# Kernel tuning notes

Measured on AMD Instinct MI355X. Metric: run time of the kernel, lower is better.

## Reference

```python
import jax, jax.numpy as jnp
from jax import lax
import numpy as np

# ---- dims / neuron params (match init_kwargs) ----
B, T, ENC, HID = 256, 500, 700, 128
TAU_MEM = 20.0      # tauSr == tauRef == tau_mem
THETA = 1.0         # spike_threshold
SCALE_REF = 1.0
WIDTH_GRAD = 1.0    # tauRho (surrogate width)
SCALE_GRAD = 1.0    # scaleRho (surrogate scale)


def alpha_filter(x, tau, mult):
    """Causal convolution along axis 0 with SLAYER's alpha (SRM) kernel
    h[k] = mult * (k/tau) * exp(1 - k/tau), Ts = 1.  Implemented as an exact
    2-state linear recurrence instead of an O(T^2) FIR conv.
    x: (T, ...) -> y: (T, ...)
    """
    d = jnp.exp(-1.0 / tau)          # per-step decay
    c = mult * jnp.exp(1.0) / tau    # h[k] = c * k * d**k

    def step(carry, xt):
        p, q = carry
        qn = d * q + c * d * p       # output at t (h[0] = 0)
        pn = d * p + xt
        return (pn, qn), qn

    z = jnp.zeros_like(x[0])
    _, y = lax.scan(step, (z, z), x)
    return y


def _spike_core(u):
    """SLAYER getSpikes: at each t, membrane = psp + accumulated refractory
    response (alpha kernel with mult = -2*theta*scaleRef, tau = tauRef) of all
    past spikes; emit spike (1/Ts) when membrane >= theta.
    u: (T, B, C) psp values -> (spikes, post-refractory membrane), both (T, B, C).
    """
    d = jnp.exp(-1.0 / TAU_MEM)
    c = (-2.0 * THETA * SCALE_REF) * jnp.exp(1.0) / TAU_MEM

    def step(carry, ut):
        p, q = carry
        qn = d * q + c * d * p       # refractory contribution at t (0 from spike at t)
        u_t = ut + qn                # membrane after refractory subtraction
        s_t = (u_t >= THETA).astype(ut.dtype)
        pn = d * p + s_t
        return (pn, qn), (s_t, u_t)

    z = jnp.zeros_like(u[0])
    _, (s, u_post) = lax.scan(step, (z, z), u)
    return s, u_post


@jax.custom_vjp
def spike(u):
    return _spike_core(u)[0]


def _spike_fwd(u):
    s, u_post = _spike_core(u)
    return s, u_post


def _spike_bwd(u_post, g):
    # SLAYER surrogate: pdf = scaleRho / (tauRho*theta) * exp(-|u - theta| / (tauRho*theta)),
    # evaluated on the refractory-modified membrane; grad does not flow through
    # the refractory recurrence (matches the torch autograd.Function).
    tc = WIDTH_GRAD * THETA
    pdf = (SCALE_GRAD / tc) * jnp.exp(-jnp.abs(u_post - THETA) / tc)
    return (g * pdf,)


spike.defvjp(_spike_fwd, _spike_bwd)


def setup_inputs():
    key = jax.random.key(0)
    k1, k2, k3 = jax.random.split(key, 3)
    # sparse binary input spike trains (B, T, ENC)
    x = (jax.random.uniform(k1, (B, T, ENC)) < 0.05).astype(jnp.float32)
    w1 = jax.random.normal(k2, (HID, ENC), dtype=jnp.float32) * 0.1
    w2 = jax.random.normal(k3, (1, HID), dtype=jnp.float32) * 0.3
    return {"x": x, "w1": w1, "w2": w2}


def reference(x, w1, w2):
    # x: (B, T, ENC) -> time-major (T, B, ENC) for the temporal scans
    xt = jnp.transpose(x, (1, 0, 2))
    h = jnp.einsum('tbc,hc->tbh', xt, w1)        # slayer.dense (bias-free linear per step)
    h = alpha_filter(h, TAU_MEM, 1.0)            # slayer.psp
    s1 = spike(h)                                # slayer.spike (threshold + refractory)
    o = jnp.einsum('tbh,oh->tbo', s1, w2)
    o = alpha_filter(o, TAU_MEM, 1.0)
    s2 = spike(o)
    return jnp.transpose(s2, (1, 0, 2))          # (B, T, 1), matches out2.movedim(-1, 1)
```

## Files before the change

### kernel.cpp

```cpp
#include <hip/hip_runtime.h>

#define BB  256
#define TT  500
#define ENC 700
#define ENC_PAD 704
#define HID 128
#define LMAX 80

__global__ __launch_bounds__(128) void transpose_w1_kernel(const float* __restrict__ w1,
                                                           float* __restrict__ w1t) {
    int c = blockIdx.x;
    int h = threadIdx.x;
    w1t[c * HID + h] = (c < ENC) ? w1[h * ENC + c] : 0.0f;
}

__global__ __launch_bounds__(256) void compress_kernel(const float* __restrict__ x,
                                                       ushort* __restrict__ lists,
                                                       int* __restrict__ ncnt) {
    __shared__ ushort lds[4][LMAX];
    const int lane = threadIdx.x & 63;
    const int w = threadIdx.x >> 6;
    const int r = blockIdx.x * 4 + w;
    const float* xrow = x + (size_t)r * ENC;
    const unsigned long long lt = (1ull << lane) - 1ull;

    float xv[11];
    #pragma unroll
    for (int k = 0; k < 11; ++k) {
        int c = k * 64 + lane;
        xv[k] = (c < ENC) ? xrow[c] : 0.0f;
    }
    int base = 0;
    #pragma unroll
    for (int k = 0; k < 11; ++k) {
        bool act = (xv[k] != 0.0f);
        unsigned long long m = __ballot(act);
        if (act) {
            int pos = base + (int)__popcll(m & lt);
            if (pos < LMAX) lds[w][pos] = (ushort)(k * 64 + lane);
        }
        base += (int)__popcll(m);
    }
    int n = (base < LMAX) ? base : LMAX;
    for (int p = n + lane; p < LMAX; p += 64) lds[w][p] = (ushort)ENC;
    if (lane == 0) ncnt[r] = n;
    if (lane < LMAX / 2)
        ((uint*)lists)[(size_t)r * (LMAX / 2) + lane] =
            ((const uint*)lds)[w * (LMAX / 2) + lane];
}

#define GROWS 512
#define GRP   64
#define QCH   16
#define WST   18

__global__ __launch_bounds__(256) void gather_kernel(const ushort* __restrict__ lists,
                                                     const int* __restrict__ ncnt,
                                                     const float* __restrict__ w1t,
                                                     float* __restrict__ h) {
    __shared__ float  w1q[ENC_PAD * WST];
    __shared__ ushort ll[GRP * LMAX];
    __shared__ int    nb[GRP];

    const int tid = threadIdx.x;
    const int lane = tid & 63;
    const int w = tid >> 6;
    const int q = blockIdx.y;
    const int r0b = blockIdx.x * GROWS;

    for (int i = tid; i < ENC_PAD * QCH; i += 256) {
        int c = i >> 4, ch = i & 15;
        w1q[c * WST + ch] = w1t[c * HID + q * QCH + ch];
    }

    const int chl = (lane & 7) * 2;
    const int rw  = lane >> 3;

    for (int g = 0; g < GROWS / GRP; ++g) {
        const int r0 = r0b + g * GRP;
        __syncthreads();
        {
            const uint* src = (const uint*)lists + (size_t)r0 * (LMAX / 2);
            uint* dst = (uint*)ll;
            #pragma unroll
            for (int k = 0; k < 10; ++k) dst[tid + k * 256] = src[tid + k * 256];
        }
        if (tid < GRP) nb[tid] = ncnt[r0 + tid];
        __syncthreads();

        #pragma unroll
        for (int p = 0; p < 2; ++p) {
            const int rl = p * 32 + w * 8 + rw;
            int n = nb[rl];
            n = max(n, __shfl_xor(n, 8));
            n = max(n, __shfl_xor(n, 16));
            n = max(n, __shfl_xor(n, 32));
            const int jmax = (n + 7) & ~7;

            float a0 = 0.f, a1 = 0.f;
            for (int j = 0; j < jmax; j += 8) {
                uint4 iv = *(const uint4*)&ll[rl * LMAX + j];
                int c0 = (int)(iv.x & 0xffff), c1 = (int)(iv.x >> 16);
                int c2 = (int)(iv.y & 0xffff), c3 = (int)(iv.y >> 16);
                int c4 = (int)(iv.z & 0xffff), c5 = (int)(iv.z >> 16);
                int c6 = (int)(iv.w & 0xffff), c7 = (int)(iv.w >> 16);
                float2 v0 = *(const float2*)&w1q[c0 * WST + chl];
                float2 v1 = *(const float2*)&w1q[c1 * WST + chl];
                float2 v2 = *(const float2*)&w1q[c2 * WST + chl];
                float2 v3 = *(const float2*)&w1q[c3 * WST + chl];
                float2 v4 = *(const float2*)&w1q[c4 * WST + chl];
                float2 v5 = *(const float2*)&w1q[c5 * WST + chl];
                float2 v6 = *(const float2*)&w1q[c6 * WST + chl];
                float2 v7 = *(const float2*)&w1q[c7 * WST + chl];
                a0 += v0.x; a1 += v0.y;
                a0 += v1.x; a1 += v1.y;
                a0 += v2.x; a1 += v2.y;
                a0 += v3.x; a1 += v3.y;
                a0 += v4.x; a1 += v4.y;
                a0 += v5.x; a1 += v5.y;
                a0 += v6.x; a1 += v6.y;
                a0 += v7.x; a1 += v7.y;
            }
            const int r = r0 + rl;
            const int b = r / TT;
            const int t = r - b * TT;
            *(float2*)&h[(size_t)t * (BB * HID) + (size_t)b * HID + q * QCH + chl] =
                make_float2(a0, a1);
        }
    }
}

__global__ __launch_bounds__(256) void spmm3_kernel(const float* __restrict__ x,
                                                    const float* __restrict__ w1t,
                                                    float* __restrict__ h) {
    __shared__ ushort lists[4][144];
    const int lane = threadIdx.x & 63;
    const int w = threadIdx.x >> 6;
    const int r = blockIdx.x * 4 + w;
    const float* xrow = x + (size_t)r * ENC;
    const unsigned long long lt = (1ull << lane) - 1ull;

    float xv[11];
    #pragma unroll
    for (int k = 0; k < 11; ++k) {
        int c = k * 64 + lane;
        xv[k] = (c < ENC) ? xrow[c] : 0.0f;
    }
    int base = 0;
    #pragma unroll
    for (int k = 0; k < 11; ++k) {
        bool act = (xv[k] != 0.0f);
        unsigned long long m = __ballot(act);
        if (act) {
            int pos = base + (int)__popcll(m & lt);
            if (pos < 128) lists[w][pos] = (ushort)(k * 64 + lane);
        }
        base += (int)__popcll(m);
    }
    int n = (base < 128) ? base : 128;
    int npad = (n + 15) & ~15;
    if (lane < npad - n) lists[w][n + lane] = (ushort)ENC;
    __syncthreads();

    float accx = 0.f, accy = 0.f;
    for (int j = 0; j < npad; j += 16) {
        int c0  = lists[w][j + 0],  c1  = lists[w][j + 1];
        int c2  = lists[w][j + 2],  c3  = lists[w][j + 3];
        int c4  = lists[w][j + 4],  c5  = lists[w][j + 5];
        int c6  = lists[w][j + 6],  c7  = lists[w][j + 7];
        int c8  = lists[w][j + 8],  c9  = lists[w][j + 9];
        int c10 = lists[w][j + 10], c11 = lists[w][j + 11];
        int c12 = lists[w][j + 12], c13 = lists[w][j + 13];
        int c14 = lists[w][j + 14], c15 = lists[w][j + 15];
        float2 t0  = ((const float2*)(w1t + (size_t)c0  * HID))[lane];
        float2 t1  = ((const float2*)(w1t + (size_t)c1  * HID))[lane];
        float2 t2  = ((const float2*)(w1t + (size_t)c2  * HID))[lane];
        float2 t3  = ((const float2*)(w1t + (size_t)c3  * HID))[lane];
        float2 t4  = ((const float2*)(w1t + (size_t)c4  * HID))[lane];
        float2 t5  = ((const float2*)(w1t + (size_t)c5  * HID))[lane];
        float2 t6  = ((const float2*)(w1t + (size_t)c6  * HID))[lane];
        float2 t7  = ((const float2*)(w1t + (size_t)c7  * HID))[lane];
        float2 t8  = ((const float2*)(w1t + (size_t)c8  * HID))[lane];
        float2 t9  = ((const float2*)(w1t + (size_t)c9  * HID))[lane];
        float2 t10 = ((const float2*)(w1t + (size_t)c10 * HID))[lane];
        float2 t11 = ((const float2*)(w1t + (size_t)c11 * HID))[lane];
        float2 t12 = ((const float2*)(w1t + (size_t)c12 * HID))[lane];
        float2 t13 = ((const float2*)(w1t + (size_t)c13 * HID))[lane];
        float2 t14 = ((const float2*)(w1t + (size_t)c14 * HID))[lane];
        float2 t15 = ((const float2*)(w1t + (size_t)c15 * HID))[lane];
        accx += t0.x;  accy += t0.y;  accx += t1.x;  accy += t1.y;
        accx += t2.x;  accy += t2.y;  accx += t3.x;  accy += t3.y;
        accx += t4.x;  accy += t4.y;  accx += t5.x;  accy += t5.y;
        accx += t6.x;  accy += t6.y;  accx += t7.x;  accy += t7.y;
        accx += t8.x;  accy += t8.y;  accx += t9.x;  accy += t9.y;
        accx += t10.x; accy += t10.y; accx += t11.x; accy += t11.y;
        accx += t12.x; accy += t12.y; accx += t13.x; accy += t13.y;
        accx += t14.x; accy += t14.y; accx += t15.x; accy += t15.y;
    }
    int b = r / TT;
    int t = r - b * TT;
    float2* dst = (float2*)(h + (size_t)t * (BB * HID) + (size_t)b * HID);
    dst[lane] = make_float2(accx, accy);
}

__global__ __launch_bounds__(128) void recur2_kernel(const float* __restrict__ hgl,
                                                     const float* __restrict__ w2,
                                                     float* __restrict__ out) {
    __shared__ float hbuf[52 * 132];
    __shared__ float vbuf[50 * 129];
    __shared__ float pbuf[2][50];

    const int b = blockIdx.x;
    const int tid = threadIdx.x;

    const float D   = 0.95122942450071400910f;
    const float CD  = (float)(0.13591409142295226 * 0.95122942450071400910);
    const float CRD = (float)(-0.27182818284590452 * 0.95122942450071400910);

    float ap = 0.f, aq = 0.f, rp = 0.f, rq = 0.f;
    float Ap = 0.f, Aq = 0.f, Rp = 0.f, Rq = 0.f;
    const float w2v = w2[tid];

    const int tl0 = tid >> 5;
    const int ch0 = (tid & 31) * 4;
    const float* hb = hgl + (size_t)b * HID + ch0;

    float4 pf[13];
    #pragma unroll
    for (int i = 0; i < 13; ++i) {
        int t = i * 4 + tl0;
        pf[i] = *(const float4*)(hb + (size_t)t * (BB * HID));
    }

    for (int chunk = 0; chunk < 10; ++chunk) {
        #pragma unroll
        for (int i = 0; i < 13; ++i)
            *(float4*)&hbuf[(i * 4 + tl0) * 132 + ch0] = pf[i];
        __syncthreads();

        {
            const int tb = (chunk + 1) * 50;
            #pragma unroll
            for (int i = 0; i < 13; ++i) {
                int t = tb + i * 4 + tl0;
                t = (t < TT) ? t : (TT - 1);
                pf[i] = *(const float4*)(hb + (size_t)t * (BB * HID));
            }
        }

        #pragma unroll
        for (int tl = 0; tl < 50; ++tl) {
            float hv = hbuf[tl * 132 + tid];
            float y = fmaf(D, aq, CD * ap);
            aq = y;
            ap = fmaf(D, ap, hv);
            float q = fmaf(D, rq, CRD * rp);
            float u = y + q;
            float s = (u >= 1.0f) ? 1.0f : 0.0f;
            rq = q;
            rp = fmaf(D, rp, s);
            vbuf[tl * 129 + tid] = s * w2v;
        }
        __syncthreads();

        if (tid < 50) {
            const float* row = &vbuf[tid * 129];
            float a0 = 0.f, a1 = 0.f, a2 = 0.f, a3 = 0.f;
            #pragma unroll
            for (int k = 0; k < 64; k += 4) {
                a0 += row[k]; a1 += row[k + 1]; a2 += row[k + 2]; a3 += row[k + 3];
            }
            pbuf[0][tid] = (a0 + a1) + (a2 + a3);
        } else if (tid >= 64 && tid < 114) {
            const float* row = &vbuf[(tid - 64) * 129 + 64];
            float a0 = 0.f, a1 = 0.f, a2 = 0.f, a3 = 0.f;
            #pragma unroll
            for (int k = 0; k < 64; k += 4) {
                a0 += row[k]; a1 += row[k + 1]; a2 += row[k + 2]; a3 += row[k + 3];
            }
            pbuf[1][tid - 64] = (a0 + a1) + (a2 + a3);
        }
        __syncthreads();

        float my_s2 = 0.f;
        #pragma unroll
        for (int tl = 0; tl < 50; ++tl) {
            float ot = pbuf[0][tl] + pbuf[1][tl];
            float y2 = fmaf(D, Aq, CD * Ap);
            Aq = y2;
            Ap = fmaf(D, Ap, ot);
            float q2 = fmaf(D, Rq, CRD * Rp);
            float u2 = y2 + q2;
            float s2 = (u2 >= 1.0f) ? 1.0f : 0.0f;
            Rq = q2;
            Rp = fmaf(D, Rp, s2);
            if (tl == tid) my_s2 = s2;
        }
        if (tid < 50) out[(size_t)b * TT + chunk * 50 + tid] = my_s2;
    }
}

extern "C" void kernel_launch(void* const* d_in, const int* in_sizes, int n_in,
                              void* d_out, int out_size, void* d_ws, size_t ws_size,
                              hipStream_t stream) {
    const float* x  = (const float*)d_in[0];
    const float* w1 = (const float*)d_in[1];
    const float* w2 = (const float*)d_in[2];
    float* out = (float*)d_out;

    const size_t H_ELEMS   = (size_t)TT * BB * HID;
    const size_t W1T_ELEMS = (size_t)ENC_PAD * HID;
    float* h   = (float*)d_ws;
    float* w1t = h + H_ELEMS;
    char* base2 = (char*)(w1t + W1T_ELEMS);
    ushort* lists = (ushort*)base2;
    int* ncnt = (int*)(base2 + (size_t)BB * TT * LMAX * 2);
    const size_t NEED = (size_t)(base2 - (char*)d_ws) +
                        (size_t)BB * TT * LMAX * 2 + (size_t)BB * TT * 4;

    hipLaunchKernelGGL(transpose_w1_kernel, dim3(ENC_PAD), dim3(HID), 0, stream, w1, w1t);
    if (ws_size >= NEED) {
        hipLaunchKernelGGL(compress_kernel, dim3((BB * TT) / 4), dim3(256), 0, stream,
                           x, lists, ncnt);
        hipLaunchKernelGGL(gather_kernel, dim3(BB * TT / GROWS, HID / QCH), dim3(256),
                           0, stream, lists, ncnt, w1t, h);
    } else {
        hipLaunchKernelGGL(spmm3_kernel, dim3((BB * TT) / 4), dim3(256), 0, stream,
                           x, w1t, h);
    }
    hipLaunchKernelGGL(recur2_kernel, dim3(BB), dim3(128), 0, stream, h, w2, out);
}
```

Measured before the change: 630.5 us.

## Store h batch-major, swizzle gather LDS, and load recurrence inputs into registers

Changes the intermediate h layout from time-major to batch-major so each recurrence block reads one contiguous slab. The recurrence kernel drops its LDS staging buffer and loads each 50-step chunk straight into registers. The gather kernel XOR-swizzles its LDS weight layout to cut bank conflicts on indexed reads. The cost is that prefetch of the next chunk no longer overlaps compute, and the register arrays raise register pressure in the recurrence kernel.

```diff
diff --git a/kernel.cpp b/kernel.cpp
--- a/kernel.cpp
+++ b/kernel.cpp
@@ -54,10 +54,14 @@
 #define QCH   16
 #define WST   18
 
-__global__ __launch_bounds__(256) void gather_kernel(const ushort* __restrict__ lists,
-                                                     const int* __restrict__ ncnt,
-                                                     const float* __restrict__ w1t,
-                                                     float* __restrict__ h) {
+__device__ __forceinline__ int swadr(int c, int k) {
+    return c * WST + 2 * (k ^ ((c >> 4) & 7));
+}
+
+__global__ __launch_bounds__(256) void gather2_kernel(const ushort* __restrict__ lists,
+                                                      const int* __restrict__ ncnt,
+                                                      const float* __restrict__ w1t,
+                                                      float* __restrict__ h) {
     __shared__ float  w1q[ENC_PAD * WST];
     __shared__ ushort ll[GRP * LMAX];
     __shared__ int    nb[GRP];
@@ -68,13 +72,14 @@
     const int q = blockIdx.y;
     const int r0b = blockIdx.x * GROWS;
 
-    for (int i = tid; i < ENC_PAD * QCH; i += 256) {
-        int c = i >> 4, ch = i & 15;
-        w1q[c * WST + ch] = w1t[c * HID + q * QCH + ch];
-    }
-
-    const int chl = (lane & 7) * 2;
-    const int rw  = lane >> 3;
+    for (int i = tid; i < ENC_PAD * 8; i += 256) {
+        int c = i >> 3, k = i & 7;
+        float2 v = *(const float2*)&w1t[c * HID + q * QCH + 2 * k];
+        *(float2*)&w1q[swadr(c, k)] = v;
+    }
+
+    const int k  = lane & 7;
+    const int rw = lane >> 3;
 
     for (int g = 0; g < GROWS / GRP; ++g) {
         const int r0 = r0b + g * GRP;
@@ -83,7 +88,7 @@
             const uint* src = (const uint*)lists + (size_t)r0 * (LMAX / 2);
             uint* dst = (uint*)ll;
             #pragma unroll
-            for (int k = 0; k < 10; ++k) dst[tid + k * 256] = src[tid + k * 256];
+            for (int kk = 0; kk < 10; ++kk) dst[tid + kk * 256] = src[tid + kk * 256];
         }
         if (tid < GRP) nb[tid] = ncnt[r0 + tid];
         __syncthreads();
@@ -104,14 +109,14 @@
                 int c2 = (int)(iv.y & 0xffff), c3 = (int)(iv.y >> 16);
                 int c4 = (int)(iv.z & 0xffff), c5 = (int)(iv.z >> 16);
                 int c6 = (int)(iv.w & 0xffff), c7 = (int)(iv.w >> 16);
-                float2 v0 = *(const float2*)&w1q[c0 * WST + chl];
-                float2 v1 = *(const float2*)&w1q[c1 * WST + chl];
-                float2 v2 = *(const float2*)&w1q[c2 * WST + chl];
-                float2 v3 = *(const float2*)&w1q[c3 * WST + chl];
-                float2 v4 = *(const float2*)&w1q[c4 * WST + chl];
-                float2 v5 = *(const float2*)&w1q[c5 * WST + chl];
-                float2 v6 = *(const float2*)&w1q[c6 * WST + chl];
-                float2 v7 = *(const float2*)&w1q[c7 * WST + chl];
+                float2 v0 = *(const float2*)&w1q[swadr(c0, k)];
+                float2 v1 = *(const float2*)&w1q[swadr(c1, k)];
+                float2 v2 = *(const float2*)&w1q[swadr(c2, k)];
+                float2 v3 = *(const float2*)&w1q[swadr(c3, k)];
+                float2 v4 = *(const float2*)&w1q[swadr(c4, k)];
+                float2 v5 = *(const float2*)&w1q[swadr(c5, k)];
+                float2 v6 = *(const float2*)&w1q[swadr(c6, k)];
+                float2 v7 = *(const float2*)&w1q[swadr(c7, k)];
                 a0 += v0.x; a1 += v0.y;
                 a0 += v1.x; a1 += v1.y;
                 a0 += v2.x; a1 += v2.y;
@@ -124,9 +129,89 @@
             const int r = r0 + rl;
             const int b = r / TT;
             const int t = r - b * TT;
-            *(float2*)&h[(size_t)t * (BB * HID) + (size_t)b * HID + q * QCH + chl] =
+            *(float2*)&h[(size_t)b * (TT * HID) + (size_t)t * HID + q * QCH + 2 * k] =
                 make_float2(a0, a1);
         }
+    }
+}
+
+__global__ __launch_bounds__(128) void recur3_kernel(const float* __restrict__ hgl,
+                                                     const float* __restrict__ w2,
+                                                     float* __restrict__ out) {
+    __shared__ float vbuf[50 * 129];
+    __shared__ float pbuf[2][50];
+
+    const int b = blockIdx.x;
+    const int tid = threadIdx.x;
+
+    const float D   = 0.95122942450071400910f;
+    const float CD  = (float)(0.13591409142295226 * 0.95122942450071400910);
+    const float CRD = (float)(-0.27182818284590452 * 0.95122942450071400910);
+
+    float ap = 0.f, aq = 0.f, rp = 0.f, rq = 0.f;
+    float Ap = 0.f, Aq = 0.f, Rp = 0.f, Rq = 0.f;
+    const float w2v = w2[tid];
+    const float* hb = hgl + (size_t)b * (TT * HID) + tid;
+
+    for (int chunk = 0; chunk < 10; ++chunk) {
+        float hv[50];
+        #pragma unroll
+        for (int tl = 0; tl < 50; ++tl)
+            hv[tl] = hb[(size_t)(chunk * 50 + tl) * HID];
+
+        #pragma unroll
+        for (int tl = 0; tl < 50; ++tl) {
+            float y = fmaf(D, aq, CD * ap);
+            aq = y;
+            ap = fmaf(D, ap, hv[tl]);
+            float qq = fmaf(D, rq, CRD * rp);
+            float u = y + qq;
+            float s = (u >= 1.0f) ? 1.0f : 0.0f;
+            rq = qq;
+            rp = fmaf(D, rp, s);
+            vbuf[tl * 129 + tid] = s * w2v;
+        }
+        __syncthreads();
+
+        if (tid < 50) {
+            const float* row = &vbuf[tid * 129];
+            float a0 = 0.f, a1 = 0.f, a2 = 0.f, a3 = 0.f;
+            #pragma unroll
+            for (int kk = 0; kk < 64; kk += 4) {
+                a0 += row[kk]; a1 += row[kk + 1]; a2 += row[kk + 2]; a3 += row[kk + 3];
+            }
+            pbuf[0][tid] = (a0 + a1) + (a2 + a3);
+        } else if (tid >= 64 && tid < 114) {
+            const float* row = &vbuf[(tid - 64) * 129 + 64];
+            float a0 = 0.f, a1 = 0.f, a2 = 0.f, a3 = 0.f;
+            #pragma unroll
+            for (int kk = 0; kk < 64; kk += 4) {
+                a0 += row[kk]; a1 += row[kk + 1]; a2 += row[kk + 2]; a3 += row[kk + 3];
+            }
+            pbuf[1][tid - 64] = (a0 + a1) + (a2 + a3);
+        }
+        __syncthreads();
+
+        float otv[50];
+        #pragma unroll
+        for (int tl = 0; tl < 50; ++tl)
+            otv[tl] = pbuf[0][tl] + pbuf[1][tl];
+
+        float my_s2 = 0.f;
+        #pragma unroll
+        for (int tl = 0; tl < 50; ++tl) {
+            float ot = otv[tl];
+            float y2 = fmaf(D, Aq, CD * Ap);
+            Aq = y2;
+            Ap = fmaf(D, Ap, ot);
+            float q2 = fmaf(D, Rq, CRD * Rp);
+            float u2 = y2 + q2;
+            float s2 = (u2 >= 1.0f) ? 1.0f : 0.0f;
+            Rq = q2;
+            Rp = fmaf(D, Rp, s2);
+            if (tl == tid) my_s2 = s2;
+        }
+        if (tid < 50) out[(size_t)b * TT + chunk * 50 + tid] = my_s2;
     }
 }
 
@@ -142,18 +227,18 @@
 
     float xv[11];
     #pragma unroll
-    for (int k = 0; k < 11; ++k) {
-        int c = k * 64 + lane;
-        xv[k] = (c < ENC) ? xrow[c] : 0.0f;
+    for (int kk = 0; kk < 11; ++kk) {
+        int c = kk * 64 + lane;
+        xv[kk] = (c < ENC) ? xrow[c] : 0.0f;
     }
     int base = 0;
     #pragma unroll
-    for (int k = 0; k < 11; ++k) {
-        bool act = (xv[k] != 0.0f);
+    for (int kk = 0; kk < 11; ++kk) {
+        bool act = (xv[kk] != 0.0f);
         unsigned long long m = __ballot(act);
         if (act) {
             int pos = base + (int)__popcll(m & lt);
-            if (pos < 128) lists[w][pos] = (ushort)(k * 64 + lane);
+            if (pos < 128) lists[w][pos] = (ushort)(kk * 64 + lane);
         }
         base += (int)__popcll(m);
     }
@@ -199,105 +284,8 @@
     }
     int b = r / TT;
     int t = r - b * TT;
-    float2* dst = (float2*)(h + (size_t)t * (BB * HID) + (size_t)b * HID);
+    float2* dst = (float2*)(h + (size_t)b * (TT * HID) + (size_t)t * HID);
     dst[lane] = make_float2(accx, accy);
-}
-
-__global__ __launch_bounds__(128) void recur2_kernel(const float* __restrict__ hgl,
-                                                     const float* __restrict__ w2,
-                                                     float* __restrict__ out) {
-    __shared__ float hbuf[52 * 132];
-    __shared__ float vbuf[50 * 129];
-    __shared__ float pbuf[2][50];
-
-    const int b = blockIdx.x;
-    const int tid = threadIdx.x;
-
-    const float D   = 0.95122942450071400910f;
-    const float CD  = (float)(0.13591409142295226 * 0.95122942450071400910);
-    const float CRD = (float)(-0.27182818284590452 * 0.95122942450071400910);
-
-    float ap = 0.f, aq = 0.f, rp = 0.f, rq = 0.f;
-    float Ap = 0.f, Aq = 0.f, Rp = 0.f, Rq = 0.f;
-    const float w2v = w2[tid];
-
-    const int tl0 = tid >> 5;
-    const int ch0 = (tid & 31) * 4;
-    const float* hb = hgl + (size_t)b * HID + ch0;
-
-    float4 pf[13];
-    #pragma unroll
-    for (int i = 0; i < 13; ++i) {
-        int t = i * 4 + tl0;
-        pf[i] = *(const float4*)(hb + (size_t)t * (BB * HID));
-    }
-
-    for (int chunk = 0; chunk < 10; ++chunk) {
-        #pragma unroll
-        for (int i = 0; i < 13; ++i)
-            *(float4*)&hbuf[(i * 4 + tl0) * 132 + ch0] = pf[i];
-        __syncthreads();
-
-        {
-            const int tb = (chunk + 1) * 50;
-            #pragma unroll
-            for (int i = 0; i < 13; ++i) {
-                int t = tb + i * 4 + tl0;
-                t = (t < TT) ? t : (TT - 1);
-                pf[i] = *(const float4*)(hb + (size_t)t * (BB * HID));
-            }
-        }
-
-        #pragma unroll
-        for (int tl = 0; tl < 50; ++tl) {
-            float hv = hbuf[tl * 132 + tid];
-            float y = fmaf(D, aq, CD * ap);
-            aq = y;
-            ap = fmaf(D, ap, hv);
-            float q = fmaf(D, rq, CRD * rp);
-            float u = y + q;
-            float s = (u >= 1.0f) ? 1.0f : 0.0f;
-            rq = q;
-            rp = fmaf(D, rp, s);
-            vbuf[tl * 129 + tid] = s * w2v;
-        }
-        __syncthreads();
-
-        if (tid < 50) {
-            const float* row = &vbuf[tid * 129];
-            float a0 = 0.f, a1 = 0.f, a2 = 0.f, a3 = 0.f;
-            #pragma unroll
-            for (int k = 0; k < 64; k += 4) {
-                a0 += row[k]; a1 += row[k + 1]; a2 += row[k + 2]; a3 += row[k + 3];
-            }
-            pbuf[0][tid] = (a0 + a1) + (a2 + a3);
-        } else if (tid >= 64 && tid < 114) {
-            const float* row = &vbuf[(tid - 64) * 129 + 64];
-            float a0 = 0.f, a1 = 0.f, a2 = 0.f, a3 = 0.f;
-            #pragma unroll
-            for (int k = 0; k < 64; k += 4) {
-                a0 += row[k]; a1 += row[k + 1]; a2 += row[k + 2]; a3 += row[k + 3];
-            }
-            pbuf[1][tid - 64] = (a0 + a1) + (a2 + a3);
-        }
-        __syncthreads();
-
-        float my_s2 = 0.f;
-        #pragma unroll
-        for (int tl = 0; tl < 50; ++tl) {
-            float ot = pbuf[0][tl] + pbuf[1][tl];
-            float y2 = fmaf(D, Aq, CD * Ap);
-            Aq = y2;
-            Ap = fmaf(D, Ap, ot);
-            float q2 = fmaf(D, Rq, CRD * Rp);
-            float u2 = y2 + q2;
-            float s2 = (u2 >= 1.0f) ? 1.0f : 0.0f;
-            Rq = q2;
-            Rp = fmaf(D, Rp, s2);
-            if (tl == tid) my_s2 = s2;
-        }
-        if (tid < 50) out[(size_t)b * TT + chunk * 50 + tid] = my_s2;
-    }
 }
 
 extern "C" void kernel_launch(void* const* d_in, const int* in_sizes, int n_in,
@@ -322,11 +310,11 @@
     if (ws_size >= NEED) {
         hipLaunchKernelGGL(compress_kernel, dim3((BB * TT) / 4), dim3(256), 0, stream,
                            x, lists, ncnt);
-        hipLaunchKernelGGL(gather_kernel, dim3(BB * TT / GROWS, HID / QCH), dim3(256),
+        hipLaunchKernelGGL(gather2_kernel, dim3(BB * TT / GROWS, HID / QCH), dim3(256),
                            0, stream, lists, ncnt, w1t, h);
     } else {
         hipLaunchKernelGGL(spmm3_kernel, dim3((BB * TT) / 4), dim3(256), 0, stream,
                            x, w1t, h);
     }
-    hipLaunchKernelGGL(recur2_kernel, dim3(BB), dim3(128), 0, stream, h, w2, out);
-}
+    hipLaunchKernelGGL(recur3_kernel, dim3(BB), dim3(128), 0, stream, h, w2, out);
+}
```

Result: slower. 656.3 us (+4.1%).
